# Performance work log

Hardware: AMD Instinct MI355X
Metric: run time of the kernel (lower is better)

Reference implementation:

```python
import jax, jax.numpy as jnp
import numpy as np

N = 50000      # nodes
E = 800000     # edges (before self-loops)
IN_DIM = 256
HID = 128
HEADS = 4
HEAD_D = HID // HEADS
LAYERS = 2
EPS = 1e-5
SLOPE = 0.2    # GATv2 leaky_relu negative slope (PyG default)


def setup_inputs() -> dict:
    key = jax.random.key(0)
    ks = jax.random.split(key, 8)
    x = jax.random.normal(ks[0], (N, IN_DIM), dtype=jnp.float32)
    edge_index = jax.random.randint(ks[1], (2, E), 0, N, dtype=jnp.int64)
    s_in = (2.0 / (IN_DIM + HID)) ** 0.5
    s_h = (2.0 / (HID + HID)) ** 0.5
    return {
        'x': x,
        'W_in': jax.random.normal(ks[2], (IN_DIM, HID), dtype=jnp.float32) * s_in,
        'b_in': jnp.zeros((HID,), jnp.float32),
        'ln_in_g': jnp.ones((HID,), jnp.float32),
        'ln_in_b': jnp.zeros((HID,), jnp.float32),
        'Wl': jax.random.normal(ks[3], (LAYERS, HID, HID), dtype=jnp.float32) * s_h,
        'Wr': jax.random.normal(ks[4], (LAYERS, HID, HID), dtype=jnp.float32) * s_h,
        'att': jax.random.normal(ks[5], (LAYERS, HEADS, HEAD_D), dtype=jnp.float32) * s_h,
        'ln_g': jnp.ones((LAYERS, HID), jnp.float32),
        'ln_b': jnp.zeros((LAYERS, HID), jnp.float32),
        'edge_index': edge_index,
    }


def layer_norm(h, g, b):
    mu = jnp.mean(h, axis=-1, keepdims=True)
    var = jnp.mean(jnp.square(h - mu), axis=-1, keepdims=True)
    return (h - mu) * jax.lax.rsqrt(var + EPS) * g + b


def gatv2_conv(h, src, dst, Wl, Wr, att):
    # h: [N, HID]; src/dst: [E'] (self-loops included)
    xl = (h @ Wl).reshape(N, HEADS, HEAD_D)   # source transform (also message)
    xr = (h @ Wr).reshape(N, HEADS, HEAD_D)   # target transform
    e = jax.nn.leaky_relu(xl[src] + xr[dst], SLOPE)          # [E', H, D]
    logits = jnp.einsum('ehd,hd->eh', e, att)                # [E', H]
    # segment softmax over incoming edges of each dst node
    m = jax.lax.stop_gradient(jax.ops.segment_max(logits, dst, num_segments=N))
    a = jnp.exp(logits - m[dst])
    z = jax.ops.segment_sum(a, dst, num_segments=N)
    alpha = a / z[dst]                                       # [E', H]
    out = jax.ops.segment_sum(xl[src] * alpha[:, :, None], dst, num_segments=N)
    return out.reshape(N, HID)


def reference(x, W_in, b_in, ln_in_g, ln_in_b, Wl, Wr, att, ln_g, ln_b, edge_index):
    loops = jnp.arange(N, dtype=edge_index.dtype)
    src = jnp.concatenate([edge_index[0], loops])
    dst = jnp.concatenate([edge_index[1], loops])
    h = jax.nn.relu(layer_norm(x @ W_in + b_in, ln_in_g, ln_in_b))
    for l in range(LAYERS):
        h_new = jax.nn.elu(layer_norm(gatv2_conv(h, src, dst, Wl[l], Wr[l], att[l]), ln_g[l], ln_b[l]))
        h = h + h_new
    return h
```

## Files before the change

kernel.cpp:

```cpp
#include <hip/hip_runtime.h>
#include <hip/hip_bf16.h>


#define NN 50000
#define EE 800000
#define EP (EE + NN)
#define IN_DIM 256
#define HID 128
#define SLOPE 0.2f
#define LN_EPS 1e-5f
#define NB 196
#define L2E 1.4426950408889634f

typedef short s8v __attribute__((ext_vector_type(8)));
typedef float f4v __attribute__((ext_vector_type(4)));

__device__ __forceinline__ float u2f(unsigned int u) {
    union { unsigned int i; float f; } c; c.i = u; return c.f;
}
__device__ __forceinline__ unsigned short f2bf(float f) {
    union { float f; unsigned int i; } c; c.f = f;
    unsigned int r = (c.i + 0x7fffu + ((c.i >> 16) & 1u)) >> 16;
    return (unsigned short)r;
}
__device__ __forceinline__ void unpack8(const uint4 raw, float* m) {
    m[0] = u2f(raw.x << 16); m[1] = u2f(raw.x & 0xffff0000u);
    m[2] = u2f(raw.y << 16); m[3] = u2f(raw.y & 0xffff0000u);
    m[4] = u2f(raw.z << 16); m[5] = u2f(raw.z & 0xffff0000u);
    m[6] = u2f(raw.w << 16); m[7] = u2f(raw.w & 0xffff0000u);
}

__global__ void prep_weights(const float* __restrict__ Win,
                             const float* __restrict__ Wl,
                             const float* __restrict__ Wr,
                             float4* __restrict__ wp) {
    const int sid = blockIdx.x * 256 + threadIdx.x;
    const float* W;
    int slot;
    if (sid < 4096) { W = Win; slot = sid; }
    else {
        const int m = (sid - 4096) >> 11;
        slot = (sid - 4096) & 2047;
        W = (m == 0) ? Wl : (m == 1) ? Wr : (m == 2) ? (Wl + 16384) : (Wr + 16384);
    }
    const int n = slot & 127;
    const int kbase = (slot >> 9) * 32 + ((slot >> 7) & 3) * 8;
    unsigned short o[8];
#pragma unroll
    for (int j = 0; j < 8; j++) o[j] = f2bf(W[(size_t)(kbase + j) * 128 + n]);
    wp[sid] = *(const float4*)o;
}

__global__ __launch_bounds__(256) void gemm_in_mfma(
        const float* __restrict__ x,
        const float4* __restrict__ wp,
        const float* __restrict__ bin,
        const float* __restrict__ g,
        const float* __restrict__ bb,
        unsigned short* __restrict__ hb) {
    __shared__ s8v wlds[4096];
    const int tid = threadIdx.x;
    const int wv = tid >> 6, lane = tid & 63;
    const int l15 = lane & 15, kseg = lane >> 4;
    const int row0 = blockIdx.x * 64 + wv * 16;
    const int arow = row0 + l15;
    const int r = (arow < NN) ? arow : 0;

    s8v afrag[8];
#pragma unroll
    for (int ks = 0; ks < 8; ks++) {
        const float* ap = x + (size_t)r * IN_DIM + ks * 32 + kseg * 8;
        const float4 a0 = *(const float4*)ap;
        const float4 a1 = *(const float4*)(ap + 4);
        unsigned short t[8] = { f2bf(a0.x), f2bf(a0.y), f2bf(a0.z), f2bf(a0.w),
                                f2bf(a1.x), f2bf(a1.y), f2bf(a1.z), f2bf(a1.w) };
        afrag[ks] = *(const s8v*)t;
    }

#pragma unroll
    for (int i = 0; i < 16; i++) {
        const int idx = i * 256 + tid;
        ((float4*)wlds)[idx] = wp[idx];
    }
    __syncthreads();

    f4v acc[8];
#pragma unroll
    for (int nb = 0; nb < 8; nb++) acc[nb] = (f4v){0.f, 0.f, 0.f, 0.f};
#pragma unroll
    for (int ks = 0; ks < 8; ks++) {
#pragma unroll
        for (int nb = 0; nb < 8; nb++) {
            const s8v bfrag = wlds[(ks * 4 + kseg) * 128 + nb * 16 + l15];
            acc[nb] = __builtin_amdgcn_mfma_f32_16x16x32_bf16(afrag[ks], bfrag, acc[nb], 0, 0, 0);
        }
    }

    float binv[8], gv[8], bbv[8];
#pragma unroll
    for (int nb = 0; nb < 8; nb++) {
        const int col = nb * 16 + l15;
        binv[nb] = bin[col]; gv[nb] = g[col]; bbv[nb] = bb[col];
    }
    float s1[4] = {0.f, 0.f, 0.f, 0.f}, s2[4] = {0.f, 0.f, 0.f, 0.f};
#pragma unroll
    for (int nb = 0; nb < 8; nb++)
#pragma unroll
        for (int reg = 0; reg < 4; reg++) {
            const float t = acc[nb][reg] + binv[nb];
            acc[nb][reg] = t;
            s1[reg] += t; s2[reg] += t * t;
        }
#pragma unroll
    for (int off = 1; off < 16; off <<= 1)
#pragma unroll
        for (int reg = 0; reg < 4; reg++) {
            s1[reg] += __shfl_xor(s1[reg], off);
            s2[reg] += __shfl_xor(s2[reg], off);
        }
    float mu[4], rstd[4];
#pragma unroll
    for (int reg = 0; reg < 4; reg++) {
        mu[reg] = s1[reg] / (float)HID;
        rstd[reg] = rsqrtf(s2[reg] / (float)HID - mu[reg] * mu[reg] + LN_EPS);
    }
    const int rbase = row0 + 4 * kseg;
#pragma unroll
    for (int reg = 0; reg < 4; reg++) {
        const int grow = rbase + reg;
        if (grow >= NN) continue;
#pragma unroll
        for (int nb = 0; nb < 8; nb++) {
            const int col = nb * 16 + l15;
            float v = (acc[nb][reg] - mu[reg]) * rstd[reg] * gv[nb] + bbv[nb];
            hb[(size_t)grow * HID + col] = f2bf(fmaxf(v, 0.f));
        }
    }
}

__global__ __launch_bounds__(256) void gemm_xlxr_mfma(
        const unsigned short* __restrict__ hb,
        const float4* __restrict__ wp,
        unsigned short* __restrict__ xl,
        unsigned short* __restrict__ xrb) {
    __shared__ s8v wlds[4096];
    const int tid = threadIdx.x;
    const int wv = tid >> 6, lane = tid & 63;
    const int l15 = lane & 15, kseg = lane >> 4;
    const int row0 = blockIdx.x * 64 + wv * 16;
    const int arow = row0 + l15;
    const int r = (arow < NN) ? arow : 0;

    s8v afrag[4];
#pragma unroll
    for (int ks = 0; ks < 4; ks++)
        afrag[ks] = *(const s8v*)(hb + (size_t)r * HID + ks * 32 + kseg * 8);

#pragma unroll
    for (int i = 0; i < 16; i++) {
        const int idx = i * 256 + tid;
        ((float4*)wlds)[idx] = wp[idx];
    }
    __syncthreads();

    f4v accL[8], accR[8];
#pragma unroll
    for (int nb = 0; nb < 8; nb++) {
        accL[nb] = (f4v){0.f, 0.f, 0.f, 0.f};
        accR[nb] = (f4v){0.f, 0.f, 0.f, 0.f};
    }
#pragma unroll
    for (int ks = 0; ks < 4; ks++) {
#pragma unroll
        for (int nb = 0; nb < 8; nb++) {
            const s8v bL = wlds[(ks * 4 + kseg) * 128 + nb * 16 + l15];
            accL[nb] = __builtin_amdgcn_mfma_f32_16x16x32_bf16(afrag[ks], bL, accL[nb], 0, 0, 0);
            const s8v bR = wlds[2048 + (ks * 4 + kseg) * 128 + nb * 16 + l15];
            accR[nb] = __builtin_amdgcn_mfma_f32_16x16x32_bf16(afrag[ks], bR, accR[nb], 0, 0, 0);
        }
    }

    const int rbase = row0 + 4 * kseg;
#pragma unroll
    for (int reg = 0; reg < 4; reg++) {
        const int grow = rbase + reg;
        if (grow >= NN) continue;
#pragma unroll
        for (int nb = 0; nb < 8; nb++) {
            const int col = nb * 16 + l15;
            xl[(size_t)grow * HID + col]  = f2bf(accL[nb][reg]);
            xrb[(size_t)grow * HID + col] = f2bf(accR[nb][reg]);
        }
    }
}

__global__ void dst_hist(const int* __restrict__ ei, int* __restrict__ cnt,
                         unsigned short* __restrict__ epos) {
    const long e = (long)blockIdx.x * 256 + threadIdx.x;
    if (e >= EP) return;
    const int d = (e < EE) ? ei[EE + e] : (int)(e - EE);
    epos[e] = (unsigned short)atomicAdd(&cnt[d], 1);
}

__global__ void scan_bsum(const int* __restrict__ cnt, int* __restrict__ bsum) {
    const int tid = threadIdx.x;
    const int i = blockIdx.x * 256 + tid;
    int v = (i < NN) ? cnt[i] : 0;
#pragma unroll
    for (int off = 1; off < 64; off <<= 1) v += __shfl_xor(v, off);
    __shared__ int ws[4];
    if ((tid & 63) == 0) ws[tid >> 6] = v;
    __syncthreads();
    if (tid == 0) bsum[blockIdx.x] = ws[0] + ws[1] + ws[2] + ws[3];
}

__global__ void scan_bpre(const int* __restrict__ bsum, int* __restrict__ bpre) {
    const int t = threadIdx.x;
    const int lane = t & 63, wv = t >> 6;
    const int v = (t < NB) ? bsum[t] : 0;
    int s = v;
#pragma unroll
    for (int off = 1; off < 64; off <<= 1) {
        const int u = __shfl_up(s, off);
        if (lane >= off) s += u;
    }
    __shared__ int wt[4];
    if (lane == 63) wt[wv] = s;
    __syncthreads();
    int add = 0;
    for (int w = 0; w < wv; w++) add += wt[w];
    if (t < NB) bpre[t] = s + add - v;
}

__global__ void scan_rowptr(const int* __restrict__ cnt,
                            const int* __restrict__ bpre,
                            int* __restrict__ rowptr) {
    const int tid = threadIdx.x;
    const int lane = tid & 63, wv = tid >> 6;
    const int i = blockIdx.x * 256 + tid;
    const int v = (i < NN) ? cnt[i] : 0;
    int s = v;
#pragma unroll
    for (int off = 1; off < 64; off <<= 1) {
        const int u = __shfl_up(s, off);
        if (lane >= off) s += u;
    }
    __shared__ int wt[4];
    if (lane == 63) wt[wv] = s;
    __syncthreads();
    int add = bpre[blockIdx.x];
    for (int w = 0; w < wv; w++) add += wt[w];
    const int excl = s + add - v;
    if (i < NN) rowptr[i] = excl;
    if (i == NN - 1) rowptr[NN] = excl + v;
}

__global__ void csr_scatter(const int* __restrict__ ei,
                            const int* __restrict__ rowptr,
                            const unsigned short* __restrict__ epos,
                            unsigned short* __restrict__ esrc16) {
    const long e = (long)blockIdx.x * 256 + threadIdx.x;
    if (e >= EP) return;
    int s, d;
    if (e < EE) { s = ei[e]; d = ei[EE + e]; }
    else        { s = d = (int)(e - EE); }
    esrc16[rowptr[d] + epos[e]] = (unsigned short)s;
}

__global__ __launch_bounds__(256) void gat_ln(
        const unsigned short* __restrict__ xl,
        const unsigned short* __restrict__ xrb,
        const float* __restrict__ att,
        const int* __restrict__ rowptr,
        const unsigned short* __restrict__ esrc16,
        const float* __restrict__ g,
        const float* __restrict__ b,
        const unsigned short* __restrict__ hres,
        float* __restrict__ dest,
        unsigned short* __restrict__ destb) {
    const int tid = threadIdx.x;
    const int lane = tid & 63;
    const int wv = tid >> 6;
    const int l16 = lane & 15;
    const int grp = lane >> 4;
    const int node = blockIdx.x * 16 + wv * 4 + grp;
    const int f0 = l16 * 8;

    float xrv[8], a06[8], a04[8];
    {
        const uint4 xraw = *(const uint4*)(xrb + (size_t)node * HID + f0);
        unpack8(xraw, xrv);
        const float4 t0 = *(const float4*)(att + f0);
        const float4 t1 = *(const float4*)(att + f0 + 4);
        float av[8] = { t0.x, t0.y, t0.z, t0.w, t1.x, t1.y, t1.z, t1.w };
#pragma unroll
        for (int j = 0; j < 8; j++) {
            a06[j] = 0.6f * L2E * av[j];
            a04[j] = 0.4f * L2E * av[j];
        }
    }
    const int beg = rowptr[node];
    const int deg = rowptr[node + 1] - beg;
    int dmax = deg;
    dmax = max(dmax, __shfl_xor(dmax, 16));
    dmax = max(dmax, __shfl_xor(dmax, 32));

    const char* xlbase = (const char*)xl + f0 * 2;
    const int gb = lane & 48;

    float acc[8];
#pragma unroll
    for (int j = 0; j < 8; j++) acc[j] = 0.f;
    float z = 0.f;

    int sb = (l16 < deg) ? (int)esrc16[beg + l16] : 0;

#define PROCR(RAW, VALID) do {                                              \
        float m[8];                                                         \
        unpack8((RAW), m);                                                  \
        float v = 0.f;                                                      \
        _Pragma("unroll")                                                   \
        for (int j = 0; j < 8; j++) {                                       \
            const float tt = m[j] + xrv[j];                                 \
            v += tt * a06[j] + fabsf(tt) * a04[j];                          \
        }                                                                   \
        v += __shfl_xor(v, 1);                                              \
        v += __shfl_xor(v, 2);                          \
        const float a = (VALID) ? __builtin_amdgcn_exp2f(v) : 0.f;          \
        z += a;                                                             \
        _Pragma("unroll")                                                   \
        for (int j = 0; j < 8; j++) acc[j] = fmaf(a, m[j], acc[j]);         \
    } while (0)

    for (int t = 0; t < dmax; t += 4) {
        if ((t & 15) == 0 && t) {
            sb = (t + l16 < deg) ? (int)esrc16[beg + t + l16] : 0;
        }
        const int o0 = __shfl(sb, gb | ((t + 0) & 15)) << 8;
        const int o1 = __shfl(sb, gb | ((t + 1) & 15)) << 8;
        const int o2 = __shfl(sb, gb | ((t + 2) & 15)) << 8;
        const int o3 = __shfl(sb, gb | ((t + 3) & 15)) << 8;
        const uint4 r0 = *(const uint4*)(xlbase + o0);
        const uint4 r1 = *(const uint4*)(xlbase + o1);
        const uint4 r2 = *(const uint4*)(xlbase + o2);
        const uint4 r3 = *(const uint4*)(xlbase + o3);
        PROCR(r0, t + 0 < deg);
        PROCR(r1, t + 1 < deg);
        PROCR(r2, t + 2 < deg);
        PROCR(r3, t + 3 < deg);
    }
#undef PROCR

    const float inv = 1.f / z;
    float o[8];
    float s1 = 0.f, s2 = 0.f;
#pragma unroll
    for (int j = 0; j < 8; j++) {
        o[j] = acc[j] * inv;
        s1 += o[j];
        s2 = fmaf(o[j], o[j], s2);
    }
#pragma unroll
    for (int off = 1; off < 16; off <<= 1) {
        s1 += __shfl_xor(s1, off);
        s2 += __shfl_xor(s2, off);
    }
    const float mu = s1 / (float)HID;
    const float rstd = rsqrtf(s2 / (float)HID - mu * mu + LN_EPS);

    float gv[8], bv[8], hv[8];
    {
        const float4 g0 = *(const float4*)(g + f0);
        const float4 g1 = *(const float4*)(g + f0 + 4);
        gv[0]=g0.x; gv[1]=g0.y; gv[2]=g0.z; gv[3]=g0.w;
        gv[4]=g1.x; gv[5]=g1.y; gv[6]=g1.z; gv[7]=g1.w;
        const float4 b0 = *(const float4*)(b + f0);
        const float4 b1 = *(const float4*)(b + f0 + 4);
        bv[0]=b0.x; bv[1]=b0.y; bv[2]=b0.z; bv[3]=b0.w;
        bv[4]=b1.x; bv[5]=b1.y; bv[6]=b1.z; bv[7]=b1.w;
        const uint4 hraw = *(const uint4*)(hres + (size_t)node * HID + f0);
        unpack8(hraw, hv);
    }
    float res[8];
#pragma unroll
    for (int j = 0; j < 8; j++) {
        float n = (o[j] - mu) * rstd * gv[j] + bv[j];
        n = (n > 0.f) ? n : (__builtin_amdgcn_exp2f(n * L2E) - 1.f);
        res[j] = hv[j] + n;
    }
    if (dest) {
        float* dp = dest + (size_t)node * HID + f0;
        *(float4*)dp       = (float4){res[0], res[1], res[2], res[3]};
        *(float4*)(dp + 4) = (float4){res[4], res[5], res[6], res[7]};
    }
    if (destb) {
        unsigned short o16[8];
#pragma unroll
        for (int j = 0; j < 8; j++) o16[j] = f2bf(res[j]);
        *(uint4*)(destb + (size_t)node * HID + f0) = *(const uint4*)o16;
    }
}

extern "C" void kernel_launch(void* const* d_in, const int* in_sizes, int n_in,
                              void* d_out, int out_size, void* d_ws, size_t ws_size,
                              hipStream_t stream) {
    const float* x       = (const float*)d_in[0];
    const float* W_in    = (const float*)d_in[1];
    const float* b_in    = (const float*)d_in[2];
    const float* ln_in_g = (const float*)d_in[3];
    const float* ln_in_b = (const float*)d_in[4];
    const float* Wl      = (const float*)d_in[5];
    const float* Wr      = (const float*)d_in[6];
    const float* att     = (const float*)d_in[7];
    const float* ln_g    = (const float*)d_in[8];
    const float* ln_b    = (const float*)d_in[9];
    const int*   ei      = (const int*)d_in[10];
    float* out = (float*)d_out;

    unsigned short* hb  = (unsigned short*)d_ws;
    unsigned short* hb2 = hb  + (size_t)NN * HID;
    unsigned short* xlb = hb2 + (size_t)NN * HID;
    unsigned short* xrb = xlb + (size_t)NN * HID;
    float4* wp = (float4*)(xrb + (size_t)NN * HID);
    int* cnt    = (int*)(wp + 12288);
    int* rowptr = cnt + NN;
    int* bsum   = rowptr + (NN + 1);
    int* bpre   = bsum + NB;
    unsigned short* epos   = (unsigned short*)(bpre + NB);
    unsigned short* esrc16 = epos + EP;

    prep_weights<<<48, 256, 0, stream>>>(W_in, Wl, Wr, wp);

    (void)hipMemsetAsync(cnt, 0, NN * sizeof(int), stream);
    const int eblocks = (EP + 255) / 256;
    dst_hist<<<eblocks, 256, 0, stream>>>(ei, cnt, epos);
    scan_bsum<<<NB, 256, 0, stream>>>(cnt, bsum);
    scan_bpre<<<1, 256, 0, stream>>>(bsum, bpre);
    scan_rowptr<<<NB, 256, 0, stream>>>(cnt, bpre, rowptr);
    csr_scatter<<<eblocks, 256, 0, stream>>>(ei, rowptr, epos, esrc16);

    const int mblocks = (NN + 63) / 64;
    gemm_in_mfma<<<mblocks, 256, 0, stream>>>(x, wp, b_in, ln_in_g, ln_in_b, hb);

    for (int l = 0; l < 2; l++) {
        const unsigned short* hsrc = (l == 0) ? hb : hb2;
        gemm_xlxr_mfma<<<mblocks, 256, 0, stream>>>(hsrc, wp + 4096 + l * 4096, xlb, xrb);
        gat_ln<<<NN / 16, 256, 0, stream>>>(xlb, xrb, att + (size_t)l * HID,
                                            rowptr, esrc16,
                                            ln_g + (size_t)l * HID,
                                            ln_b + (size_t)l * HID,
                                            hsrc,
                                            (l == 1) ? out : (float*)nullptr,
                                            (l == 0) ? hb2 : (unsigned short*)nullptr);
    }
}
```

Before: 188.1 us.

## Fold block-prefix scan into rowptr kernel, prefetch edge indices, use DPP quad sums

```diff
diff --git a/kernel.cpp b/kernel.cpp
--- a/kernel.cpp
+++ b/kernel.cpp
@@ -28,6 +28,13 @@
     m[2] = u2f(raw.y << 16); m[3] = u2f(raw.y & 0xffff0000u);
     m[4] = u2f(raw.z << 16); m[5] = u2f(raw.z & 0xffff0000u);
     m[6] = u2f(raw.w << 16); m[7] = u2f(raw.w & 0xffff0000u);
+}
+__device__ __forceinline__ float quad_sum(float v) {
+    v += __int_as_float(__builtin_amdgcn_update_dpp(
+            0, __float_as_int(v), 0xB1 , 0xF, 0xF, true));
+    v += __int_as_float(__builtin_amdgcn_update_dpp(
+            0, __float_as_int(v), 0x4E , 0xF, 0xF, true));
+    return v;
 }
 
 __global__ void prep_weights(const float* __restrict__ Win,
@@ -214,10 +221,26 @@
     if (tid == 0) bsum[blockIdx.x] = ws[0] + ws[1] + ws[2] + ws[3];
 }
 
-__global__ void scan_bpre(const int* __restrict__ bsum, int* __restrict__ bpre) {
-    const int t = threadIdx.x;
-    const int lane = t & 63, wv = t >> 6;
-    const int v = (t < NB) ? bsum[t] : 0;
+__global__ void scan_rowptr(const int* __restrict__ cnt,
+                            const int* __restrict__ bsum,
+                            int* __restrict__ rowptr) {
+    const int tid = threadIdx.x;
+    const int lane = tid & 63, wv = tid >> 6;
+    __shared__ int ws[4];
+    __shared__ int pref;
+
+    {
+        int v = (tid < blockIdx.x && tid < NB) ? bsum[tid] : 0;
+#pragma unroll
+        for (int off = 1; off < 64; off <<= 1) v += __shfl_xor(v, off);
+        if (lane == 0) ws[wv] = v;
+        __syncthreads();
+        if (tid == 0) pref = ws[0] + ws[1] + ws[2] + ws[3];
+        __syncthreads();
+    }
+
+    const int i = blockIdx.x * 256 + tid;
+    const int v = (i < NN) ? cnt[i] : 0;
     int s = v;
 #pragma unroll
     for (int off = 1; off < 64; off <<= 1) {
@@ -227,28 +250,7 @@
     __shared__ int wt[4];
     if (lane == 63) wt[wv] = s;
     __syncthreads();
-    int add = 0;
-    for (int w = 0; w < wv; w++) add += wt[w];
-    if (t < NB) bpre[t] = s + add - v;
-}
-
-__global__ void scan_rowptr(const int* __restrict__ cnt,
-                            const int* __restrict__ bpre,
-                            int* __restrict__ rowptr) {
-    const int tid = threadIdx.x;
-    const int lane = tid & 63, wv = tid >> 6;
-    const int i = blockIdx.x * 256 + tid;
-    const int v = (i < NN) ? cnt[i] : 0;
-    int s = v;
-#pragma unroll
-    for (int off = 1; off < 64; off <<= 1) {
-        const int u = __shfl_up(s, off);
-        if (lane >= off) s += u;
-    }
-    __shared__ int wt[4];
-    if (lane == 63) wt[wv] = s;
-    __syncthreads();
-    int add = bpre[blockIdx.x];
+    int add = pref;
     for (int w = 0; w < wv; w++) add += wt[w];
     const int excl = s + add - v;
     if (i < NN) rowptr[i] = excl;
@@ -313,7 +315,8 @@
     for (int j = 0; j < 8; j++) acc[j] = 0.f;
     float z = 0.f;
 
-    int sb = (l16 < deg) ? (int)esrc16[beg + l16] : 0;
+    int sb_cur = (l16 < deg)      ? (int)esrc16[beg + l16]      : 0;
+    int sb_nxt = (16 + l16 < deg) ? (int)esrc16[beg + 16 + l16] : 0;
 
 #define PROCR(RAW, VALID) do {                                              \
         float m[8];                                                         \
@@ -324,8 +327,7 @@
             const float tt = m[j] + xrv[j];                                 \
             v += tt * a06[j] + fabsf(tt) * a04[j];                          \
         }                                                                   \
-        v += __shfl_xor(v, 1);                                              \
-        v += __shfl_xor(v, 2);                          \
+        v = quad_sum(v);                           \
         const float a = (VALID) ? __builtin_amdgcn_exp2f(v) : 0.f;          \
         z += a;                                                             \
         _Pragma("unroll")                                                   \
@@ -334,12 +336,13 @@
 
     for (int t = 0; t < dmax; t += 4) {
         if ((t & 15) == 0 && t) {
-            sb = (t + l16 < deg) ? (int)esrc16[beg + t + l16] : 0;
-        }
-        const int o0 = __shfl(sb, gb | ((t + 0) & 15)) << 8;
-        const int o1 = __shfl(sb, gb | ((t + 1) & 15)) << 8;
-        const int o2 = __shfl(sb, gb | ((t + 2) & 15)) << 8;
-        const int o3 = __shfl(sb, gb | ((t + 3) & 15)) << 8;
+            sb_cur = sb_nxt;
+            sb_nxt = (t + 16 + l16 < deg) ? (int)esrc16[beg + t + 16 + l16] : 0;
+        }
+        const int o0 = __shfl(sb_cur, gb | ((t + 0) & 15)) << 8;
+        const int o1 = __shfl(sb_cur, gb | ((t + 1) & 15)) << 8;
+        const int o2 = __shfl(sb_cur, gb | ((t + 2) & 15)) << 8;
+        const int o3 = __shfl(sb_cur, gb | ((t + 3) & 15)) << 8;
         const uint4 r0 = *(const uint4*)(xlbase + o0);
         const uint4 r1 = *(const uint4*)(xlbase + o1);
         const uint4 r2 = *(const uint4*)(xlbase + o2);
@@ -425,8 +428,7 @@
     int* cnt    = (int*)(wp + 12288);
     int* rowptr = cnt + NN;
     int* bsum   = rowptr + (NN + 1);
-    int* bpre   = bsum + NB;
-    unsigned short* epos   = (unsigned short*)(bpre + NB);
+    unsigned short* epos   = (unsigned short*)(bsum + NB);
     unsigned short* esrc16 = epos + EP;
 
     prep_weights<<<48, 256, 0, stream>>>(W_in, Wl, Wr, wp);
@@ -435,8 +437,7 @@
     const int eblocks = (EP + 255) / 256;
     dst_hist<<<eblocks, 256, 0, stream>>>(ei, cnt, epos);
     scan_bsum<<<NB, 256, 0, stream>>>(cnt, bsum);
-    scan_bpre<<<1, 256, 0, stream>>>(bsum, bpre);
-    scan_rowptr<<<NB, 256, 0, stream>>>(cnt, bpre, rowptr);
+    scan_rowptr<<<NB, 256, 0, stream>>>(cnt, bsum, rowptr);
     csr_scatter<<<eblocks, 256, 0, stream>>>(ei, rowptr, epos, esrc16);
 
     const int mblocks = (NN + 63) / 64;
```

Result: faster. 183.2 us (-2.6%).
